# Performance work log

Measured on AMD Instinct MI355X. Metric: run time of the kernel, lower is better.

## Reference

```python
import jax, jax.numpy as jnp
import numpy as np

B, T, C, H = 2, 2048, 1024, 16
HD = C // H  # head dim = 64


def setup_inputs() -> dict:
    key = jax.random.key(0)
    ks = jax.random.split(key, 5)
    scale = 0.02
    return {
        "x": jax.random.normal(ks[0], (B, T, C), dtype=jnp.float32),
        "W_attn": jax.random.normal(ks[1], (C, 3 * C), dtype=jnp.float32) * scale,
        "b_attn": jax.random.normal(ks[2], (3 * C,), dtype=jnp.float32) * scale,
        "W_proj": jax.random.normal(ks[3], (C, C), dtype=jnp.float32) * scale,
        "b_proj": jax.random.normal(ks[4], (C,), dtype=jnp.float32) * scale,
    }


def reference(x, W_attn, b_attn, W_proj, b_proj):
    Bd, Td, Cd = x.shape
    qkv = x @ W_attn + b_attn                      # [B,T,3C]
    q, k, v = jnp.split(qkv, 3, axis=-1)           # each [B,T,C]
    # [B,T,C] -> [B,H,T,HD]
    def heads(t):
        return t.reshape(Bd, Td, H, HD).transpose(0, 2, 1, 3)
    q, k, v = heads(q), heads(k), heads(v)
    att = jnp.einsum('bhqd,bhkd->bhqk', q, k) * (1.0 / np.sqrt(HD))
    causal = jnp.tril(jnp.ones((Td, Td), dtype=bool))
    att = jnp.where(causal[None, None, :, :], att, -jnp.inf)
    att = jax.nn.softmax(att, axis=-1)
    y = jnp.einsum('bhqk,bhkd->bhqd', att, v)      # [B,H,T,HD]
    y = y.transpose(0, 2, 1, 3).reshape(Bd, Td, Cd)
    return y @ W_proj + b_proj
```

## Files before the change

### kernel.cpp

```cpp
#include <hip/hip_runtime.h>
#include <hip/hip_bf16.h>


typedef __attribute__((ext_vector_type(8))) __bf16 bf16x8;
typedef __attribute__((ext_vector_type(8))) short short8;
typedef __attribute__((ext_vector_type(4))) short short4v;
typedef __attribute__((ext_vector_type(4))) float floatx4;

__device__ __forceinline__ unsigned short f2b(float f) {
    unsigned int x = __float_as_uint(f);
    x += 0x7fffu + ((x >> 16) & 1u);
    return (unsigned short)(x >> 16);
}
__device__ __forceinline__ unsigned short f2b_trunc(float f) {
    return (unsigned short)(__float_as_uint(f) >> 16);
}
__device__ __forceinline__ void gld16(const void* g, void* l) {
    __builtin_amdgcn_global_load_lds((const __attribute__((address_space(1))) void*)g,
                                     (__attribute__((address_space(3))) void*)l, 16, 0, 0);
}

__global__ __launch_bounds__(256) void cvt_k(
    const float* __restrict__ in, unsigned short* __restrict__ out, int n)
{
    int i = (blockIdx.x * 256 + threadIdx.x) << 3;
    if (i >= n) return;
    const float4 a = *(const float4*)(in + i);
    const float4 b = *(const float4*)(in + i + 4);
    short8 v;
    v[0] = (short)f2b(a.x); v[1] = (short)f2b(a.y);
    v[2] = (short)f2b(a.z); v[3] = (short)f2b(a.w);
    v[4] = (short)f2b(b.x); v[5] = (short)f2b(b.y);
    v[6] = (short)f2b(b.z); v[7] = (short)f2b(b.w);
    *(short8*)(out + i) = v;
}

__global__ __launch_bounds__(256) void transpose_cvt_k(
    const float* __restrict__ in, unsigned short* __restrict__ out,
    int R, int Cc)
{
    __shared__ unsigned short tl[64][72];
    const int t = threadIdx.x;
    const int r0 = blockIdx.y * 64, c0 = blockIdx.x * 64;
#pragma unroll
    for (int it = 0; it < 2; ++it) {
        int idx = it * 256 + t, r = idx >> 3, c8 = (idx & 7) << 3;
        const float* p = in + (size_t)(r0 + r) * Cc + c0 + c8;
        const float4 a = *(const float4*)p;
        const float4 b = *(const float4*)(p + 4);
        tl[r][c8 + 0] = f2b(a.x); tl[r][c8 + 1] = f2b(a.y);
        tl[r][c8 + 2] = f2b(a.z); tl[r][c8 + 3] = f2b(a.w);
        tl[r][c8 + 4] = f2b(b.x); tl[r][c8 + 5] = f2b(b.y);
        tl[r][c8 + 6] = f2b(b.z); tl[r][c8 + 7] = f2b(b.w);
    }
    __syncthreads();
#pragma unroll
    for (int it = 0; it < 2; ++it) {
        int idx = it * 256 + t, rr = idx >> 3, c8 = (idx & 7) << 3;
        short8 v;
#pragma unroll
        for (int i = 0; i < 8; ++i) v[i] = (short)tl[c8 + i][rr];
        *(short8*)(out + (size_t)(c0 + rr) * R + r0 + c8) = v;
    }
}

__global__ __launch_bounds__(256) void gemm_bt(
    const unsigned short* __restrict__ A,
    const unsigned short* __restrict__ BT,
    const float* __restrict__ bias,
    unsigned short* __restrict__ outqk,
    unsigned short* __restrict__ outvt,
    float* __restrict__ outf,
    int M, int N, int K, int mode)
{
    __shared__ unsigned short Ald[128][32];
    __shared__ unsigned short Bld[128][32];

    const int t = threadIdx.x;
    const int w = t >> 6, lane = t & 63, l15 = lane & 15, quad = lane >> 4;
    const int wr = w >> 1, wc = w & 1;
    const int m0 = blockIdx.y * 128, n0 = blockIdx.x * 128;

    floatx4 acc[4][4];
#pragma unroll
    for (int i = 0; i < 4; ++i)
#pragma unroll
        for (int j = 0; j < 4; ++j) acc[i][j] = (floatx4)0.f;

    const int row_s = t >> 2, kg_s = (t & 3) << 3;
    for (int k0 = 0; k0 < K; k0 += 32) {
        __syncthreads();
#pragma unroll
        for (int c = 0; c < 2; ++c) {
            int row = c * 64 + row_s;
            const unsigned short* ga = A  + (size_t)(m0 + row) * K + k0 + kg_s;
            const unsigned short* gb = BT + (size_t)(n0 + row) * K + k0 + kg_s;
            gld16(ga, &Ald[0][0] + (size_t)(c * 256 + w * 64) * 8);
            gld16(gb, &Bld[0][0] + (size_t)(c * 256 + w * 64) * 8);
        }
        __syncthreads();

        bf16x8 af[4], bfr[4];
#pragma unroll
        for (int i = 0; i < 4; ++i) af[i] = *(const bf16x8*)&Ald[wr * 64 + i * 16 + l15][quad * 8];
#pragma unroll
        for (int j = 0; j < 4; ++j) bfr[j] = *(const bf16x8*)&Bld[wc * 64 + j * 16 + l15][quad * 8];
#pragma unroll
        for (int i = 0; i < 4; ++i)
#pragma unroll
            for (int j = 0; j < 4; ++j)
                acc[i][j] = __builtin_amdgcn_mfma_f32_16x16x32_bf16(af[i], bfr[j], acc[i][j], 0, 0, 0);
    }

#pragma unroll
    for (int j = 0; j < 4; ++j) {
        int col = n0 + wc * 64 + j * 16 + l15;
        float bia = bias[col];
        int which = col >> 10, c = col & 1023;
        int h = c >> 6, d = c & 63;
#pragma unroll
        for (int i = 0; i < 4; ++i) {
            int rb = m0 + wr * 64 + i * 16 + quad * 4;
            if (mode == 0) {
#pragma unroll
                for (int r = 0; r < 4; ++r)
                    outf[(size_t)(rb + r) * N + col] = acc[i][j][r] + bia;
            } else {
                int b = rb >> 11, tt = rb & 2047;
                if (which == 2) {
                    short4v pk;
#pragma unroll
                    for (int r = 0; r < 4; ++r) pk[r] = (short)f2b(acc[i][j][r] + bia);
                    *(short4v*)(outvt + ((size_t)((b << 4) + h) * 64 + d) * 2048 + tt) = pk;
                } else {
                    unsigned short* base = outqk + (size_t)which * 4194304
                                         + (((size_t)((b << 4) + h) * 2048 + tt) * 64 + d);
#pragma unroll
                    for (int r = 0; r < 4; ++r) base[(size_t)r * 64] = f2b(acc[i][j][r] + bia);
                }
            }
        }
    }
}

__global__ __launch_bounds__(256) void attn_k(
    const unsigned short* __restrict__ qg,
    const unsigned short* __restrict__ kg,
    const unsigned short* __restrict__ vt,
    unsigned short* __restrict__ y)
{
    __shared__ unsigned short Kb[2][64][64];
    __shared__ unsigned short Vb[2][64][64];
    __shared__ unsigned short Pld[4][16][72];

    const int t = threadIdx.x, w = t >> 6, lane = t & 63;
    const int l15 = lane & 15, quad = lane >> 4;
    const int bh = blockIdx.x >> 4, p = blockIdx.x & 15;
    const int b = bh >> 4, h = bh & 15;
    const float SC = 0.18033688011112042f;

    bf16x8 ones;
#pragma unroll
    for (int i = 0; i < 8; ++i) ones[i] = (__bf16)1.0f;

    const int r_s = t >> 3;
    const int g_s = t & 7;

#pragma unroll 1
    for (int hv = 0; hv < 2; ++hv) {
        const int qt = hv ? (31 - p) : p;
        const int qbase = qt * 64;

        bf16x8 qa[2];
        {
            const unsigned short* qrow = qg + ((size_t)bh * 2048 + qbase + w * 16 + l15) * 64;
            qa[0] = *(const bf16x8*)(qrow + quad * 8);
            qa[1] = *(const bf16x8*)(qrow + 32 + quad * 8);
        }

        floatx4 O[4];
#pragma unroll
        for (int j = 0; j < 4; ++j) O[j] = (floatx4)0.f;
        floatx4 lacc = (floatx4)0.f;

        __syncthreads();
        {
            const int kbase = 0;
#pragma unroll
            for (int c = 0; c < 2; ++c) {
                int r = c * 32 + r_s;
                int cg = (g_s ^ (r & 7)) << 3;
                gld16(kg + ((size_t)bh * 2048 + kbase + r) * 64 + cg,
                      &Kb[0][0][0] + (size_t)(c * 256 + w * 64) * 8);
                gld16(vt + ((size_t)bh * 64 + r) * 2048 + kbase + cg,
                      &Vb[0][0][0] + (size_t)(c * 256 + w * 64) * 8);
            }
        }

#pragma unroll 1
        for (int kt = 0; kt <= qt; ++kt) {
            __syncthreads();
            const int cur = kt & 1;
            if (kt < qt) {
                const int kbase = (kt + 1) * 64, nxt = cur ^ 1;
#pragma unroll
                for (int c = 0; c < 2; ++c) {
                    int r = c * 32 + r_s;
                    int cg = (g_s ^ (r & 7)) << 3;
                    gld16(kg + ((size_t)bh * 2048 + kbase + r) * 64 + cg,
                          &Kb[nxt][0][0] + (size_t)(c * 256 + w * 64) * 8);
                    gld16(vt + ((size_t)bh * 64 + r) * 2048 + kbase + cg,
                          &Vb[nxt][0][0] + (size_t)(c * 256 + w * 64) * 8);
                }
            }

            floatx4 sv[4];
#pragma unroll
            for (int jn = 0; jn < 4; ++jn) sv[jn] = (floatx4)0.f;
#pragma unroll
            for (int kk = 0; kk < 2; ++kk) {
#pragma unroll
                for (int jn = 0; jn < 4; ++jn) {
                    bf16x8 bfr = *(const bf16x8*)&Kb[cur][jn * 16 + l15][((kk * 4 + quad) ^ (l15 & 7)) << 3];
                    sv[jn] = __builtin_amdgcn_mfma_f32_16x16x32_bf16(qa[kk], bfr, sv[jn], 0, 0, 0);
                }
            }

            if (kt == qt) {
#pragma unroll
                for (int jn = 0; jn < 4; ++jn) {
                    int key = jn * 16 + l15;
#pragma unroll
                    for (int r = 0; r < 4; ++r) {
                        int qr = w * 16 + quad * 4 + r;
                        float s = (key > qr) ? -1e30f : sv[jn][r];
                        sv[jn][r] = exp2f(s * SC);
                    }
                }
            } else {
#pragma unroll
                for (int jn = 0; jn < 4; ++jn)
#pragma unroll
                    for (int r = 0; r < 4; ++r) sv[jn][r] = exp2f(sv[jn][r] * SC);
            }

#pragma unroll
            for (int jn = 0; jn < 4; ++jn)
#pragma unroll
                for (int r = 0; r < 4; ++r)
                    Pld[w][quad * 4 + r][jn * 16 + l15] = f2b_trunc(sv[jn][r]);
            __builtin_amdgcn_wave_barrier();
            __builtin_amdgcn_s_waitcnt(0xc07f);
            __builtin_amdgcn_wave_barrier();

#pragma unroll
            for (int kk = 0; kk < 2; ++kk) {
                bf16x8 pa = *(const bf16x8*)&Pld[w][l15][kk * 32 + quad * 8];
                lacc = __builtin_amdgcn_mfma_f32_16x16x32_bf16(pa, ones, lacc, 0, 0, 0);
#pragma unroll
                for (int jd = 0; jd < 4; ++jd) {
                    bf16x8 vb = *(const bf16x8*)&Vb[cur][jd * 16 + l15][((kk * 4 + quad) ^ (l15 & 7)) << 3];
                    O[jd] = __builtin_amdgcn_mfma_f32_16x16x32_bf16(pa, vb, O[jd], 0, 0, 0);
                }
            }
        }

#pragma unroll
        for (int r = 0; r < 4; ++r) {
            float inv = 1.f / lacc[r];
            int tt = qbase + w * 16 + quad * 4 + r;
#pragma unroll
            for (int jd = 0; jd < 4; ++jd) {
                int c = h * 64 + jd * 16 + l15;
                y[((size_t)b * 2048 + tt) * 1024 + c] = f2b(O[jd][r] * inv);
            }
        }
    }
}

extern "C" void kernel_launch(void* const* d_in, const int* in_sizes, int n_in,
                              void* d_out, int out_size, void* d_ws, size_t ws_size,
                              hipStream_t stream) {
    const float* x      = (const float*)d_in[0];
    const float* W_attn = (const float*)d_in[1];
    const float* b_attn = (const float*)d_in[2];
    const float* W_proj = (const float*)d_in[3];
    const float* b_proj = (const float*)d_in[4];
    float* out = (float*)d_out;

    char* ws = (char*)d_ws;
    unsigned short* qk  = (unsigned short*)(ws);
    unsigned short* vtb = (unsigned short*)(ws + 16777216);
    unsigned short* y   = (unsigned short*)(ws + 25165824);
    unsigned short* xb  = (unsigned short*)(ws + 33554432);
    unsigned short* WTa = (unsigned short*)(ws + 41943040);
    unsigned short* WTp = (unsigned short*)(ws + 48234496);

    cvt_k<<<2048, 256, 0, stream>>>(x, xb, 4194304);
    transpose_cvt_k<<<dim3(48, 16), 256, 0, stream>>>(W_attn, WTa, 1024, 3072);
    transpose_cvt_k<<<dim3(16, 16), 256, 0, stream>>>(W_proj, WTp, 1024, 1024);
    gemm_bt<<<dim3(24, 32), 256, 0, stream>>>(xb, WTa, b_attn, qk, vtb, nullptr, 4096, 3072, 1024, 1);
    attn_k<<<512, 256, 0, stream>>>(qk, qk + 4194304, vtb, y);
    gemm_bt<<<dim3(8, 32), 256, 0, stream>>>(y, WTp, b_proj, nullptr, nullptr, out, 4096, 1024, 1024, 0);
}
```

Measured before the change: 204.9 us.

## Stage GEMM epilogues through LDS for coalesced stores; shrink proj tile

Splits the generic GEMM into a QKV kernel and a projection kernel. Both now stage their epilogue through shared memory so global writes become 16-byte coalesced rows instead of scattered 2-byte or 4-byte stores. The V transpose is also done inside LDS. The projection GEMM moves to 128x64 tiles, doubling its block count from 256 to 512 to fill the GPU better. In exchange this adds extra LDS usage and barriers, and only one wave-group writes at a time during the epilogue.

```diff
diff --git a/kernel.cpp b/kernel.cpp
--- a/kernel.cpp
+++ b/kernel.cpp
@@ -64,22 +64,26 @@
     }
 }
 
-__global__ __launch_bounds__(256) void gemm_bt(
+__global__ __launch_bounds__(256) void gemm_qkv(
     const unsigned short* __restrict__ A,
     const unsigned short* __restrict__ BT,
     const float* __restrict__ bias,
     unsigned short* __restrict__ outqk,
-    unsigned short* __restrict__ outvt,
-    float* __restrict__ outf,
-    int M, int N, int K, int mode)
+    unsigned short* __restrict__ outvt)
 {
     __shared__ unsigned short Ald[128][32];
     __shared__ unsigned short Bld[128][32];
+    __shared__ __align__(16) unsigned short Esc[128 * 72];
 
     const int t = threadIdx.x;
     const int w = t >> 6, lane = t & 63, l15 = lane & 15, quad = lane >> 4;
     const int wr = w >> 1, wc = w & 1;
     const int m0 = blockIdx.y * 128, n0 = blockIdx.x * 128;
+    const int K = 1024;
+
+    float bia[4];
+#pragma unroll
+    for (int j = 0; j < 4; ++j) bia[j] = bias[n0 + wc * 64 + j * 16 + l15];
 
     floatx4 acc[4][4];
 #pragma unroll
@@ -93,10 +97,8 @@
 #pragma unroll
         for (int c = 0; c < 2; ++c) {
             int row = c * 64 + row_s;
-            const unsigned short* ga = A  + (size_t)(m0 + row) * K + k0 + kg_s;
-            const unsigned short* gb = BT + (size_t)(n0 + row) * K + k0 + kg_s;
-            gld16(ga, &Ald[0][0] + (size_t)(c * 256 + w * 64) * 8);
-            gld16(gb, &Bld[0][0] + (size_t)(c * 256 + w * 64) * 8);
+            gld16(A  + (size_t)(m0 + row) * K + k0 + kg_s, &Ald[0][0] + (size_t)(c * 256 + w * 64) * 8);
+            gld16(BT + (size_t)(n0 + row) * K + k0 + kg_s, &Bld[0][0] + (size_t)(c * 256 + w * 64) * 8);
         }
         __syncthreads();
 
@@ -112,34 +114,125 @@
                 acc[i][j] = __builtin_amdgcn_mfma_f32_16x16x32_bf16(af[i], bfr[j], acc[i][j], 0, 0, 0);
     }
 
-#pragma unroll
-    for (int j = 0; j < 4; ++j) {
-        int col = n0 + wc * 64 + j * 16 + l15;
-        float bia = bias[col];
-        int which = col >> 10, c = col & 1023;
-        int h = c >> 6, d = c & 63;
-#pragma unroll
-        for (int i = 0; i < 4; ++i) {
-            int rb = m0 + wr * 64 + i * 16 + quad * 4;
-            if (mode == 0) {
-#pragma unroll
-                for (int r = 0; r < 4; ++r)
-                    outf[(size_t)(rb + r) * N + col] = acc[i][j][r] + bia;
-            } else {
-                int b = rb >> 11, tt = rb & 2047;
-                if (which == 2) {
-                    short4v pk;
-#pragma unroll
-                    for (int r = 0; r < 4; ++r) pk[r] = (short)f2b(acc[i][j][r] + bia);
-                    *(short4v*)(outvt + ((size_t)((b << 4) + h) * 64 + d) * 2048 + tt) = pk;
-                } else {
-                    unsigned short* base = outqk + (size_t)which * 4194304
-                                         + (((size_t)((b << 4) + h) * 2048 + tt) * 64 + d);
-#pragma unroll
-                    for (int r = 0; r < 4; ++r) base[(size_t)r * 64] = f2b(acc[i][j][r] + bia);
-                }
-            }
-        }
+    const int bb = m0 >> 11, tbase = m0 & 2047;
+    if (n0 < 2048) {
+        for (int cf = 0; cf < 2; ++cf) {
+            __syncthreads();
+            if (wc == cf) {
+#pragma unroll
+                for (int i = 0; i < 4; ++i)
+#pragma unroll
+                    for (int j = 0; j < 4; ++j)
+#pragma unroll
+                        for (int r = 0; r < 4; ++r)
+                            Esc[(wr * 64 + i * 16 + quad * 4 + r) * 72 + j * 16 + l15] =
+                                f2b(acc[i][j][r] + bia[j]);
+            }
+            __syncthreads();
+            const int fb = n0 + cf * 64;
+            const int which = fb >> 10, h = (fb & 1023) >> 6;
+            const int row = t >> 1, co = (t & 1) << 5;
+            const unsigned short* src = Esc + row * 72 + co;
+            unsigned short* dst = outqk + (size_t)which * 4194304
+                + (((size_t)(bb * 16 + h) * 2048 + tbase + row) * 64 + co);
+#pragma unroll
+            for (int u = 0; u < 4; ++u)
+                *(short8*)(dst + u * 8) = *(const short8*)(src + u * 8);
+        }
+    } else {
+        const int hb = (n0 & 1023) >> 6;
+        for (int hf = 0; hf < 2; ++hf) {
+            __syncthreads();
+            if (wr == hf) {
+#pragma unroll
+                for (int i = 0; i < 4; ++i)
+#pragma unroll
+                    for (int j = 0; j < 4; ++j) {
+                        short4v pk;
+#pragma unroll
+                        for (int r = 0; r < 4; ++r) pk[r] = (short)f2b(acc[i][j][r] + bia[j]);
+                        *(short4v*)&Esc[(wc * 64 + j * 16 + l15) * 72 + i * 16 + quad * 4] = pk;
+                    }
+            }
+            __syncthreads();
+            const int dl = t >> 1, co = (t & 1) << 5;
+            const int h = hb + (dl >> 6), d = dl & 63;
+            const unsigned short* src = Esc + dl * 72 + co;
+            unsigned short* dst = outvt
+                + (((size_t)(bb * 16 + h) * 64 + d) * 2048 + tbase + hf * 64 + co);
+#pragma unroll
+            for (int u = 0; u < 4; ++u)
+                *(short8*)(dst + u * 8) = *(const short8*)(src + u * 8);
+        }
+    }
+}
+
+__global__ __launch_bounds__(256) void gemm_proj(
+    const unsigned short* __restrict__ A,
+    const unsigned short* __restrict__ BT,
+    const float* __restrict__ bias,
+    float* __restrict__ outf)
+{
+    __shared__ unsigned short Ald[128][32];
+    __shared__ unsigned short Bld[64][32];
+    __shared__ __align__(16) float Ef[32 * 68];
+
+    const int t = threadIdx.x;
+    const int w = t >> 6, lane = t & 63, l15 = lane & 15, quad = lane >> 4;
+    const int m0 = blockIdx.y * 128, n0 = blockIdx.x * 64;
+    const int K = 1024, N = 1024;
+
+    float bia[4];
+#pragma unroll
+    for (int j = 0; j < 4; ++j) bia[j] = bias[n0 + j * 16 + l15];
+
+    floatx4 acc[2][4];
+#pragma unroll
+    for (int i = 0; i < 2; ++i)
+#pragma unroll
+        for (int j = 0; j < 4; ++j) acc[i][j] = (floatx4)0.f;
+
+    const int row_s = t >> 2, kg_s = (t & 3) << 3;
+    for (int k0 = 0; k0 < K; k0 += 32) {
+        __syncthreads();
+#pragma unroll
+        for (int c = 0; c < 2; ++c)
+            gld16(A + (size_t)(m0 + c * 64 + row_s) * K + k0 + kg_s,
+                  &Ald[0][0] + (size_t)(c * 256 + w * 64) * 8);
+        gld16(BT + (size_t)(n0 + row_s) * K + k0 + kg_s,
+              &Bld[0][0] + (size_t)(w * 64) * 8);
+        __syncthreads();
+
+        bf16x8 af[2], bfr[4];
+#pragma unroll
+        for (int i = 0; i < 2; ++i) af[i] = *(const bf16x8*)&Ald[w * 32 + i * 16 + l15][quad * 8];
+#pragma unroll
+        for (int j = 0; j < 4; ++j) bfr[j] = *(const bf16x8*)&Bld[j * 16 + l15][quad * 8];
+#pragma unroll
+        for (int i = 0; i < 2; ++i)
+#pragma unroll
+            for (int j = 0; j < 4; ++j)
+                acc[i][j] = __builtin_amdgcn_mfma_f32_16x16x32_bf16(af[i], bfr[j], acc[i][j], 0, 0, 0);
+    }
+
+    for (int qf = 0; qf < 4; ++qf) {
+        __syncthreads();
+        if (w == qf) {
+#pragma unroll
+            for (int i = 0; i < 2; ++i)
+#pragma unroll
+                for (int j = 0; j < 4; ++j)
+#pragma unroll
+                    for (int r = 0; r < 4; ++r)
+                        Ef[(i * 16 + quad * 4 + r) * 68 + j * 16 + l15] = acc[i][j][r] + bia[j];
+        }
+        __syncthreads();
+        const int row = t >> 3, co = (t & 7) << 3;
+        const float* src = Ef + row * 68 + co;
+        float* dst = outf + (size_t)(m0 + qf * 32 + row) * N + n0 + co;
+#pragma unroll
+        for (int u = 0; u < 2; ++u)
+            *(float4*)(dst + u * 4) = *(const float4*)(src + u * 4);
     }
 }
 
@@ -185,14 +278,13 @@
 
         __syncthreads();
         {
-            const int kbase = 0;
 #pragma unroll
             for (int c = 0; c < 2; ++c) {
                 int r = c * 32 + r_s;
                 int cg = (g_s ^ (r & 7)) << 3;
-                gld16(kg + ((size_t)bh * 2048 + kbase + r) * 64 + cg,
+                gld16(kg + ((size_t)bh * 2048 + r) * 64 + cg,
                       &Kb[0][0][0] + (size_t)(c * 256 + w * 64) * 8);
-                gld16(vt + ((size_t)bh * 64 + r) * 2048 + kbase + cg,
+                gld16(vt + ((size_t)bh * 64 + r) * 2048 + cg,
                       &Vb[0][0][0] + (size_t)(c * 256 + w * 64) * 8);
             }
         }
@@ -299,7 +391,7 @@
     cvt_k<<<2048, 256, 0, stream>>>(x, xb, 4194304);
     transpose_cvt_k<<<dim3(48, 16), 256, 0, stream>>>(W_attn, WTa, 1024, 3072);
     transpose_cvt_k<<<dim3(16, 16), 256, 0, stream>>>(W_proj, WTp, 1024, 1024);
-    gemm_bt<<<dim3(24, 32), 256, 0, stream>>>(xb, WTa, b_attn, qk, vtb, nullptr, 4096, 3072, 1024, 1);
+    gemm_qkv<<<dim3(24, 32), 256, 0, stream>>>(xb, WTa, b_attn, qk, vtb);
     attn_k<<<512, 256, 0, stream>>>(qk, qk + 4194304, vtb, y);
-    gemm_bt<<<dim3(8, 32), 256, 0, stream>>>(y, WTp, b_proj, nullptr, nullptr, out, 4096, 1024, 1024, 0);
-}
+    gemm_proj<<<dim3(16, 32), 256, 0, stream>>>(y, WTp, b_proj, out);
+}
```

Measured after the change: 209.3 us. +2.2%, slower.
